# Kernel tuning notes

Hardware: AMD Instinct MI355X
Metric: run time of the kernel (lower is better)

## Reference

```python
import jax, jax.numpy as jnp
import numpy as np

S, L, K = 4, 256, 32          # num_states, seq length, neighbors
ORIG_H, EMB_H, EXV, RANK = 128, 256, 384, 16


def _integrate(x, Wq, Wk, seq_idx, emb_idx, hidden, rank):
    """AttentionIntegrator.forward: QK^T softmax -> double mean -> softmax -> weighted pool of raw x."""
    x = jnp.moveaxis(x, (seq_idx, emb_idx), (-2, -1))
    orig_shape = x.shape
    Ls = orig_shape[-2]
    xf = x.reshape(-1, Ls, hidden)               # (B, Ls, hidden)
    B = xf.shape[0]
    q = (xf @ Wq.T).reshape(B, Ls, rank, hidden)  # head_dim == hidden
    k = (xf @ Wk.T).reshape(B, Ls, rank, hidden)
    scale = 1.0 / jnp.sqrt(jnp.asarray(hidden, xf.dtype))
    scores = jnp.einsum('blhd,bmhd->bhlm', q, k) * scale
    attn = jax.nn.softmax(scores, axis=-1)        # (B, rank, Ls, Ls)
    w = jax.nn.softmax(attn.mean(axis=(1, 2)), axis=-1)  # (B, Ls)
    pooled = jnp.einsum('bl,bld->bd', w, xf)      # (B, hidden)
    return (pooled.reshape(*orig_shape[:-2], hidden),
            w.reshape(*orig_shape[:-2], Ls))


def setup_inputs() -> dict:
    key = jax.random.key(0)
    ks = jax.random.split(key, 12)
    sc = lambda fan_in: 1.0 / np.sqrt(fan_in)
    return {
        'h_V':    jax.random.normal(ks[0], (S, L, ORIG_H), jnp.float32),
        'h_EXV':  jax.random.normal(ks[1], (S, L, K, EXV), jnp.float32),
        'W_hV':   jax.random.normal(ks[2], (EMB_H, ORIG_H), jnp.float32) * sc(ORIG_H),
        'b_hV':   jnp.zeros((EMB_H,), jnp.float32),
        'Wq_hv':  jax.random.normal(ks[3], (RANK * EMB_H, EMB_H), jnp.float32) * sc(EMB_H),
        'Wk_hv':  jax.random.normal(ks[4], (RANK * EMB_H, EMB_H), jnp.float32) * sc(EMB_H),
        'Wq_ce':  jax.random.normal(ks[5], (RANK * EXV, EXV), jnp.float32) * sc(EXV),
        'Wk_ce':  jax.random.normal(ks[6], (RANK * EXV, EXV), jnp.float32) * sc(EXV),
        'W_ce':   jax.random.normal(ks[7], (EMB_H, EXV), jnp.float32) * sc(EXV),
        'b_ce':   jnp.zeros((EMB_H,), jnp.float32),
        'Wq_sce': jax.random.normal(ks[8], (RANK * EMB_H, EMB_H), jnp.float32) * sc(EMB_H),
        'Wk_sce': jax.random.normal(ks[9], (RANK * EMB_H, EMB_H), jnp.float32) * sc(EMB_H),
    }


def reference(h_V, h_EXV, W_hV, b_hV, Wq_hv, Wk_hv, Wq_ce, Wk_ce, W_ce, b_ce, Wq_sce, Wk_sce):
    # diffmodel.get_weights
    hv = h_V @ W_hV.T + b_hV                                  # (S, L, EMB_H)
    h_V_int, h_V_w = _integrate(hv, Wq_hv, Wk_hv, 0, 2, EMB_H, RANK)   # pool over states
    # chemical environment: pool over k neighbors per (state, position)
    ce, _local_w = _integrate(h_EXV, Wq_ce, Wk_ce, 2, 3, EXV, RANK)    # (S, L, EXV)
    ce = ce @ W_ce.T + b_ce                                   # (S, L, EMB_H)
    ce_int, ce_w = _integrate(ce, Wq_sce, Wk_sce, 0, 2, EMB_H, RANK)   # pool over states
    return (h_V_int[None], h_V_w[None], ce_int[None], ce_w[None])
```

## Files before the change

kernel.cpp:

```cpp
#include <hip/hip_runtime.h>

typedef _Float16 f16;
typedef _Float16 f16x8 __attribute__((ext_vector_type(8)));
typedef _Float16 f16x4 __attribute__((ext_vector_type(4)));
typedef float f32x4 __attribute__((ext_vector_type(4)));

#define MFMA16(a, b, c) __builtin_amdgcn_mfma_f32_16x16x32_f16(a, b, c, 0, 0, 0)
#define MFMA16K16(a, b, c) __builtin_amdgcn_mfma_f32_16x16x16f16(a, b, c, 0, 0, 0)

__global__ __launch_bounds__(256) void k_mt3(const float* __restrict__ Wq_hv,
                                             const float* __restrict__ Wk_hv,
                                             f16* __restrict__ mt_hv,
                                             const float* __restrict__ Wq_ce,
                                             const float* __restrict__ Wk_ce,
                                             f16* __restrict__ mt_ce,
                                             const float* __restrict__ Wq_sce,
                                             const float* __restrict__ Wk_sce,
                                             f16* __restrict__ mt_sce) {
    const int y = blockIdx.y;
    const float *Wq, *Wk;
    f16* MT;
    int H, ty;
    if (y < 16)      { Wq = Wq_hv;  Wk = Wk_hv;  MT = mt_hv;  H = 256; ty = y; }
    else if (y < 52) { Wq = Wq_ce;  Wk = Wk_ce;  MT = mt_ce;  H = 384; ty = y - 16; }
    else             { Wq = Wq_sce; Wk = Wk_sce; MT = mt_sce; H = 256; ty = y - 52; }

    const int h = blockIdx.x;
    const int ntile = H >> 6;
    const int nkk = H >> 5;
    const int frow = (ty / ntile) * 64;
    const int ecol = (ty % ntile) * 64;
    const int t = threadIdx.x;
    const int lane = t & 63;
    const int w = t >> 6;
    const int wr = w >> 1, wc = w & 1;

    __shared__ __align__(16) f16 As[64][40];
    __shared__ __align__(16) f16 Ks[64][40];

    f32x4 acc[2][2] = {};
    const int d = t >> 3;
    const int e8 = (t & 7) * 8;

    for (int kk = 0; kk < nkk; ++kk) {
        const float* gq = Wq + (size_t)(h * H + kk * 32 + d) * H + ecol + e8;
        const float* gk = Wk + (size_t)(h * H + kk * 32 + d) * H + frow + e8;
        float q[8], k[8];
#pragma unroll
        for (int i = 0; i < 8; ++i) { q[i] = gq[i]; k[i] = gk[i]; }
        __syncthreads();
#pragma unroll
        for (int i = 0; i < 8; ++i) { As[e8 + i][d] = (f16)q[i]; Ks[e8 + i][d] = (f16)k[i]; }
        __syncthreads();
        f16x8 a[2], b[2];
#pragma unroll
        for (int rt = 0; rt < 2; ++rt)
            a[rt] = *(const f16x8*)&Ks[wr * 32 + rt * 16 + (lane & 15)][(lane >> 4) * 8];
#pragma unroll
        for (int nt = 0; nt < 2; ++nt)
            b[nt] = *(const f16x8*)&As[wc * 32 + nt * 16 + (lane & 15)][(lane >> 4) * 8];
#pragma unroll
        for (int rt = 0; rt < 2; ++rt)
#pragma unroll
            for (int nt = 0; nt < 2; ++nt)
                acc[rt][nt] = MFMA16(a[rt], b[nt], acc[rt][nt]);
    }
#pragma unroll
    for (int rt = 0; rt < 2; ++rt)
#pragma unroll
        for (int nt = 0; nt < 2; ++nt)
#pragma unroll
            for (int j = 0; j < 4; ++j) {
                int f = frow + wr * 32 + rt * 16 + (lane >> 4) * 4 + j;
                int e = ecol + wc * 32 + nt * 16 + (lane & 15);
                MT[(((size_t)h * nkk + (e >> 5)) * H + f) * 32 + (e & 31)] = (f16)acc[rt][nt][j];
            }
}

__global__ __launch_bounds__(256) void k_lin(const float* __restrict__ in,
                                             const float* __restrict__ W,
                                             const float* __restrict__ bias,
                                             float* __restrict__ out, int K) {
    const int t = threadIdx.x;
    const int r0 = blockIdx.x * 4;
    __shared__ float ins[4][384];
    __shared__ float Ws[256][33];
#pragma unroll
    for (int r = 0; r < 4; ++r)
        for (int off = t; off < K; off += 256)
            ins[r][off] = in[(size_t)(r0 + r) * K + off];
    float acc[4] = {};
    for (int d0 = 0; d0 < K; d0 += 32) {
        __syncthreads();
        for (int i = t; i < 256 * 32; i += 256) {
            int j = i >> 5, dd = i & 31;
            Ws[j][dd] = W[(size_t)j * K + d0 + dd];
        }
        __syncthreads();
#pragma unroll 8
        for (int dd = 0; dd < 32; ++dd) {
            float wv = Ws[t][dd];
#pragma unroll
            for (int r = 0; r < 4; ++r) acc[r] += wv * ins[r][d0 + dd];
        }
    }
    float bv = bias[t];
#pragma unroll
    for (int r = 0; r < 4; ++r) out[(size_t)(r0 + r) * 256 + t] = acc[r] + bv;
}

__global__ __launch_bounds__(256) void k_small_int(const float* __restrict__ X,
                                                   const f16* __restrict__ MT,
                                                   float* __restrict__ wpart) {
    const int t = threadIdx.x;
    const int lane = t & 63;
    const int w = t >> 6;
    const int g = lane >> 4;
    const int l15 = lane & 15;
    const int pos0 = blockIdx.x * 8;
    const int h = blockIdx.y;

    __shared__ __align__(16) f16 Xs[32][264];
    __shared__ __align__(16) f16 Ts[32][264];

    {
        int row = t >> 3, d0 = (t & 7) * 32;
        int s = row & 3, p = row >> 2;
        const float* gx = X + (size_t)(s * 256 + pos0 + p) * 256 + d0;
#pragma unroll
        for (int i = 0; i < 32; i += 8) {
            float4 v0 = *(const float4*)(gx + i);
            float4 v1 = *(const float4*)(gx + i + 4);
            f16x8 o;
            o[0] = (f16)v0.x; o[1] = (f16)v0.y; o[2] = (f16)v0.z; o[3] = (f16)v0.w;
            o[4] = (f16)v1.x; o[5] = (f16)v1.y; o[6] = (f16)v1.z; o[7] = (f16)v1.w;
            *(f16x8*)&Xs[row][d0 + i] = o;
        }
    }
    __syncthreads();

    const f16* mh = MT + (size_t)h * 8 * 256 * 32;
    const int fb = w * 64 + l15;
    f32x4 acc[2][4] = {};
    f16x8 bq[4], bn[4];
#pragma unroll
    for (int nt = 0; nt < 4; ++nt)
        bq[nt] = *(const f16x8*)(mh + (size_t)(fb + nt * 16) * 32 + g * 8);
#pragma unroll
    for (int kk = 0; kk < 8; ++kk) {
        if (kk < 7) {
#pragma unroll
            for (int nt = 0; nt < 4; ++nt)
                bn[nt] = *(const f16x8*)(mh + ((size_t)(kk + 1) * 256 + fb + nt * 16) * 32 + g * 8);
        }
        f16x8 a[2];
#pragma unroll
        for (int mt = 0; mt < 2; ++mt)
            a[mt] = *(const f16x8*)&Xs[mt * 16 + l15][kk * 32 + g * 8];
#pragma unroll
        for (int mt = 0; mt < 2; ++mt)
#pragma unroll
            for (int nt = 0; nt < 4; ++nt)
                acc[mt][nt] = MFMA16(a[mt], bq[nt], acc[mt][nt]);
#pragma unroll
        for (int nt = 0; nt < 4; ++nt) bq[nt] = bn[nt];
    }
#pragma unroll
    for (int mt = 0; mt < 2; ++mt)
#pragma unroll
        for (int nt = 0; nt < 4; ++nt)
#pragma unroll
            for (int j = 0; j < 4; ++j)
                Ts[mt * 16 + g * 4 + j][w * 64 + nt * 16 + l15] = (f16)acc[mt][nt][j];
    __syncthreads();

    if (w < 2) {
        f32x4 sacc = {};
#pragma unroll
        for (int ks = 0; ks < 8; ++ks) {
            f16x8 a = *(const f16x8*)&Ts[w * 16 + l15][ks * 32 + g * 8];
            f16x8 b = *(const f16x8*)&Xs[w * 16 + l15][ks * 32 + g * 8];
            sacc = MFMA16(a, b, sacc);
        }
        if ((l15 >> 2) == g) {
            const float scale = 1.0f / 16.0f;
            float add = 0.f;
#pragma unroll
            for (int j = 0; j < 4; ++j) {
                float v = sacc[j] * scale;
                float m = v;
                m = fmaxf(m, __shfl_xor(m, 1));
                m = fmaxf(m, __shfl_xor(m, 2));
                float e = expf(v - m);
                float s2 = e;
                s2 += __shfl_xor(s2, 1);
                s2 += __shfl_xor(s2, 2);
                add += e / s2;
            }
            int pg = pos0 + w * 4 + g;
            wpart[((size_t)h * 256 + pg) * 4 + (l15 & 3)] = add;
        }
    }
}

__global__ __launch_bounds__(256) void k_small_fin(const float* __restrict__ wpart,
                                                   const float* __restrict__ X,
                                                   float* __restrict__ out_int,
                                                   float* __restrict__ out_w) {
    const int pos = blockIdx.x, t = threadIdx.x;
    __shared__ float red[64];
    __shared__ float ws[4];
    if (t < 64) red[t] = wpart[((size_t)(t >> 2) * 256 + pos) * 4 + (t & 3)];
    __syncthreads();
    if (t == 0) {
        float v[4];
#pragma unroll
        for (int s = 0; s < 4; ++s) {
            float x = 0.f;
            for (int hh = 0; hh < 16; ++hh) x += red[hh * 4 + s];
            v[s] = x * (1.0f / 64.0f);
        }
        float m = fmaxf(fmaxf(v[0], v[1]), fmaxf(v[2], v[3]));
        float sum = 0.f;
#pragma unroll
        for (int s = 0; s < 4; ++s) { v[s] = expf(v[s] - m); sum += v[s]; }
#pragma unroll
        for (int s = 0; s < 4; ++s) ws[s] = v[s] / sum;
    }
    __syncthreads();
    if (t < 4) out_w[pos * 4 + t] = ws[t];
    float v = 0.f;
#pragma unroll
    for (int s = 0; s < 4; ++s) v += ws[s] * X[(size_t)(s * 256 + pos) * 256 + t];
    out_int[(size_t)pos * 256 + t] = v;
}

#define BUF_OFF 98304

__global__ __launch_bounds__(512, 2) void k_ce_int(const float* __restrict__ Xg32,
                                                   const f16* __restrict__ MT,
                                                   float* __restrict__ acc_out) {
    const int t = threadIdx.x;
    const int lane = t & 63;
    const int w = t >> 6;
    const int g = lane >> 4;
    const int l15 = lane & 15;
    const int bg = blockIdx.x;

    extern __shared__ __align__(16) char smem[];
    char* BUF = smem + BUF_OFF;

    {
        const float* xg = Xg32 + (size_t)bg * 128 * 384;
#pragma unroll
        for (int p = 0; p < 12; ++p) {
            int idx = p * 512 + t;
            int row = idx / 48, s = idx - row * 48;
            int c = s ^ (row & 7);
            const float* src = xg + row * 384 + c * 8;
            float4 v0 = *(const float4*)src;
            float4 v1 = *(const float4*)(src + 4);
            f16x8 o;
            o[0] = (f16)v0.x; o[1] = (f16)v0.y; o[2] = (f16)v0.z; o[3] = (f16)v0.w;
            o[4] = (f16)v1.x; o[5] = (f16)v1.y; o[6] = (f16)v1.z; o[7] = (f16)v1.w;
            *(f16x8*)(smem + idx * 16) = o;
        }
    }
    __syncthreads();

    const f16* mall = MT;
    const int frow = w * 48 + l15;

    f16x8 A[3][3];
#pragma unroll
    for (int ft = 0; ft < 3; ++ft) {
        A[0][ft] = *(const f16x8*)(mall + (size_t)(frow + ft * 16) * 32 + g * 8);
        A[1][ft] = *(const f16x8*)(mall + (size_t)12288 + (size_t)(frow + ft * 16) * 32 + g * 8);
    }

    for (int hi = 0; hi < 16; ++hi) {
        f32x4 acc[3][8] = {};
#pragma unroll
        for (int kk = 0; kk < 12; ++kk) {
            {
                int step = hi * 12 + kk + 2;
                int ns = step < 192 ? step : 191;
#pragma unroll
                for (int ft = 0; ft < 3; ++ft)
                    A[(kk + 2) % 3][ft] =
                        *(const f16x8*)(mall + (size_t)ns * 12288 + (size_t)(frow + ft * 16) * 32 + g * 8);
            }
            f16x8 xb[8];
#pragma unroll
            for (int mt = 0; mt < 8; ++mt) {
                int row = mt * 16 + l15;
                int ch = kk * 4 + g;
                xb[mt] = *(const f16x8*)(smem + row * 768 + ((ch ^ (row & 7)) << 4));
            }
            __builtin_amdgcn_s_setprio(1);
#pragma unroll
            for (int ft = 0; ft < 3; ++ft)
#pragma unroll
                for (int mt = 0; mt < 8; ++mt)
                    acc[ft][mt] = MFMA16(A[kk % 3][ft], xb[mt], acc[ft][mt]);
            __builtin_amdgcn_s_setprio(0);
        }

        f16x4 bf[3][8];
#pragma unroll
        for (int ft = 0; ft < 3; ++ft)
#pragma unroll
            for (int mt = 0; mt < 8; ++mt) {
                f32x4 v = acc[ft][mt];
                f16x4 o;
                o[0] = (f16)v[0]; o[1] = (f16)v[1]; o[2] = (f16)v[2]; o[3] = (f16)v[3];
                bf[ft][mt] = o;
            }

#pragma unroll
        for (int r = 0; r < 2; ++r) {
            f32x4 s2[2][2][2] = {};
#pragma unroll
            for (int bb = 0; bb < 2; ++bb) {
                const int b = 2 * r + bb;
#pragma unroll
                for (int ks = 0; ks < 3; ++ks)
#pragma unroll
                    for (int it = 0; it < 2; ++it) {
                        int row = b * 32 + it * 16 + l15;
                        int ch = 6 * w + 2 * ks + (g >> 1);
                        f16x4 av = *(const f16x4*)(smem + row * 768 +
                                                   ((ch ^ (row & 7)) << 4) + 8 * (g & 1));
#pragma unroll
                        for (int lt = 0; lt < 2; ++lt)
                            s2[bb][it][lt] = MFMA16K16(av, bf[ks][2 * b + lt], s2[bb][it][lt]);
                    }
            }
#pragma unroll
            for (int bb = 0; bb < 2; ++bb)
#pragma unroll
                for (int it = 0; it < 2; ++it)
#pragma unroll
                    for (int lt = 0; lt < 2; ++lt)
                        *(f32x4*)(BUF + w * 8192 + (bb * 4 + it * 2 + lt) * 1024 + lane * 16) =
                            s2[bb][it][lt];
            __syncthreads();

            if ((w >> 2) == r) {
                const int wl = w & 3;
                const int bb = wl >> 1;
                const int it = wl & 1;
                const int b = 2 * r + bb;
                f32x4 sum0 = {0.f, 0.f, 0.f, 0.f};
                f32x4 sum1 = {0.f, 0.f, 0.f, 0.f};
#pragma unroll
                for (int src = 0; src < 8; ++src) {
                    const char* pb = BUF + src * 8192 + (bb * 4 + it * 2) * 1024 + lane * 16;
                    sum0 += *(const f32x4*)pb;
                    sum1 += *(const f32x4*)(pb + 1024);
                }
                const float scale = 0.051031036307982884f;
                float cs0 = 0.f, cs1 = 0.f;
#pragma unroll
                for (int j = 0; j < 4; ++j) {
                    float v0 = sum0[j] * scale, v1 = sum1[j] * scale;
                    float m = fmaxf(v0, v1);
                    m = fmaxf(m, __shfl_xor(m, 1));
                    m = fmaxf(m, __shfl_xor(m, 2));
                    m = fmaxf(m, __shfl_xor(m, 4));
                    m = fmaxf(m, __shfl_xor(m, 8));
                    float e0 = expf(v0 - m), e1 = expf(v1 - m);
                    float s = e0 + e1;
                    s += __shfl_xor(s, 1);
                    s += __shfl_xor(s, 2);
                    s += __shfl_xor(s, 4);
                    s += __shfl_xor(s, 8);
                    float inv = 1.f / s;
                    cs0 += e0 * inv;
                    cs1 += e1 * inv;
                }
                cs0 += __shfl_xor(cs0, 16); cs0 += __shfl_xor(cs0, 32);
                cs1 += __shfl_xor(cs1, 16); cs1 += __shfl_xor(cs1, 32);
                if (lane < 16) {
                    float* o = acc_out + (((size_t)hi * 1024 + bg * 4 + b) * 2 + it) * 32;
                    o[l15] = cs0;
                    o[16 + l15] = cs1;
                }
            }
            __syncthreads();
        }
    }
}

__global__ __launch_bounds__(128) void k_ce_pool(const float* __restrict__ accp,
                                                 const float* __restrict__ exv,
                                                 float* __restrict__ pooled) {
    const int b = blockIdx.x;
    const int t = threadIdx.x;
    __shared__ float wm[32];
    __shared__ float ww[32];
    if (t < 32) {
        float s = 0.f;
#pragma unroll
        for (int h = 0; h < 16; ++h) {
            s += accp[(((size_t)h * 1024 + b) * 2 + 0) * 32 + t];
            s += accp[(((size_t)h * 1024 + b) * 2 + 1) * 32 + t];
        }
        wm[t] = s * (1.0f / 512.0f);
    }
    __syncthreads();
    if (t == 0) {
        float m = wm[0];
        for (int i = 1; i < 32; ++i) m = fmaxf(m, wm[i]);
        float s = 0.f;
        for (int i = 0; i < 32; ++i) { float e = expf(wm[i] - m); ww[i] = e; s += e; }
        float inv = 1.f / s;
        for (int i = 0; i < 32; ++i) ww[i] *= inv;
    }
    __syncthreads();
    for (int d = t; d < 384; d += 128) {
        float v = 0.f;
#pragma unroll
        for (int m = 0; m < 32; ++m) v += ww[m] * exv[((size_t)b * 32 + m) * 384 + d];
        pooled[(size_t)b * 384 + d] = v;
    }
}

extern "C" void kernel_launch(void* const* d_in, const int* in_sizes, int n_in,
                              void* d_out, int out_size, void* d_ws, size_t ws_size,
                              hipStream_t stream) {
    const float* h_V    = (const float*)d_in[0];
    const float* h_EXV  = (const float*)d_in[1];
    const float* W_hV   = (const float*)d_in[2];
    const float* b_hV   = (const float*)d_in[3];
    const float* Wq_hv  = (const float*)d_in[4];
    const float* Wk_hv  = (const float*)d_in[5];
    const float* Wq_ce  = (const float*)d_in[6];
    const float* Wk_ce  = (const float*)d_in[7];
    const float* W_ce   = (const float*)d_in[8];
    const float* b_ce   = (const float*)d_in[9];
    const float* Wq_sce = (const float*)d_in[10];
    const float* Wk_sce = (const float*)d_in[11];
    float* out = (float*)d_out;

    char* ws = (char*)d_ws;
    f16*   mt_hv  = (f16*)(ws + 0);
    f16*   mt_sce = (f16*)(ws + 2097152);
    f16*   mt_ce  = (f16*)(ws + 4194304);
    float* hv     = (float*)(ws + 8912896);
    float* ce     = (float*)(ws + 9961472);
    float* accp   = (float*)(ws + 11010048);
    float* pooled = (float*)(ws + 15204352);
    float* wpart  = accp;

    k_mt3<<<dim3(16, 68), 256, 0, stream>>>(Wq_hv, Wk_hv, mt_hv,
                                            Wq_ce, Wk_ce, mt_ce,
                                            Wq_sce, Wk_sce, mt_sce);
    k_lin<<<256, 256, 0, stream>>>(h_V, W_hV, b_hV, hv, 128);
    k_small_int<<<dim3(32, 16), 256, 0, stream>>>(hv, mt_hv, wpart);
    k_small_fin<<<256, 256, 0, stream>>>(wpart, hv, out + 0, out + 65536);
    k_ce_int<<<dim3(256), 512, 163840, stream>>>(h_EXV, mt_ce, accp);
    k_ce_pool<<<1024, 128, 0, stream>>>(accp, h_EXV, pooled);
    k_lin<<<256, 256, 0, stream>>>(pooled, W_ce, b_ce, ce, 384);
    k_small_int<<<dim3(32, 16), 256, 0, stream>>>(ce, mt_sce, wpart);
    k_small_fin<<<256, 256, 0, stream>>>(wpart, ce, out + 66560, out + 132096);
}
```

Before: 301.9 us.

## Halve ce_int tile to 64 rows, store partial scores in fp16, double grid

```diff
diff --git a/kernel.cpp b/kernel.cpp
--- a/kernel.cpp
+++ b/kernel.cpp
@@ -235,7 +235,7 @@
     out_int[(size_t)pos * 256 + t] = v;
 }
 
-#define BUF_OFF 98304
+#define BUF_OFF 49152
 
 __global__ __launch_bounds__(512, 2) void k_ce_int(const float* __restrict__ Xg32,
                                                    const f16* __restrict__ MT,
@@ -251,9 +251,9 @@
     char* BUF = smem + BUF_OFF;
 
     {
-        const float* xg = Xg32 + (size_t)bg * 128 * 384;
-#pragma unroll
-        for (int p = 0; p < 12; ++p) {
+        const float* xg = Xg32 + (size_t)bg * 64 * 384;
+#pragma unroll
+        for (int p = 0; p < 6; ++p) {
             int idx = p * 512 + t;
             int row = idx / 48, s = idx - row * 48;
             int c = s ^ (row & 7);
@@ -279,7 +279,7 @@
     }
 
     for (int hi = 0; hi < 16; ++hi) {
-        f32x4 acc[3][8] = {};
+        f32x4 acc[3][4] = {};
 #pragma unroll
         for (int kk = 0; kk < 12; ++kk) {
             {
@@ -290,9 +290,9 @@
                     A[(kk + 2) % 3][ft] =
                         *(const f16x8*)(mall + (size_t)ns * 12288 + (size_t)(frow + ft * 16) * 32 + g * 8);
             }
-            f16x8 xb[8];
-#pragma unroll
-            for (int mt = 0; mt < 8; ++mt) {
+            f16x8 xb[4];
+#pragma unroll
+            for (int mt = 0; mt < 4; ++mt) {
                 int row = mt * 16 + l15;
                 int ch = kk * 4 + g;
                 xb[mt] = *(const f16x8*)(smem + row * 768 + ((ch ^ (row & 7)) << 4));
@@ -301,75 +301,69 @@
 #pragma unroll
             for (int ft = 0; ft < 3; ++ft)
 #pragma unroll
-                for (int mt = 0; mt < 8; ++mt)
+                for (int mt = 0; mt < 4; ++mt)
                     acc[ft][mt] = MFMA16(A[kk % 3][ft], xb[mt], acc[ft][mt]);
             __builtin_amdgcn_s_setprio(0);
         }
 
-        f16x4 bf[3][8];
+        f16x4 bf[3][4];
 #pragma unroll
         for (int ft = 0; ft < 3; ++ft)
 #pragma unroll
-            for (int mt = 0; mt < 8; ++mt) {
+            for (int mt = 0; mt < 4; ++mt) {
                 f32x4 v = acc[ft][mt];
                 f16x4 o;
                 o[0] = (f16)v[0]; o[1] = (f16)v[1]; o[2] = (f16)v[2]; o[3] = (f16)v[3];
                 bf[ft][mt] = o;
             }
 
+        const float scale = 0.051031036307982884f;
+
 #pragma unroll
         for (int r = 0; r < 2; ++r) {
-            f32x4 s2[2][2][2] = {};
-#pragma unroll
-            for (int bb = 0; bb < 2; ++bb) {
-                const int b = 2 * r + bb;
-#pragma unroll
-                for (int ks = 0; ks < 3; ++ks)
-#pragma unroll
-                    for (int it = 0; it < 2; ++it) {
-                        int row = b * 32 + it * 16 + l15;
-                        int ch = 6 * w + 2 * ks + (g >> 1);
-                        f16x4 av = *(const f16x4*)(smem + row * 768 +
-                                                   ((ch ^ (row & 7)) << 4) + 8 * (g & 1));
-#pragma unroll
-                        for (int lt = 0; lt < 2; ++lt)
-                            s2[bb][it][lt] = MFMA16K16(av, bf[ks][2 * b + lt], s2[bb][it][lt]);
-                    }
-            }
-#pragma unroll
-            for (int bb = 0; bb < 2; ++bb)
-#pragma unroll
-                for (int it = 0; it < 2; ++it)
+            f32x4 s2[2][2] = {};
+#pragma unroll
+            for (int ks = 0; ks < 3; ++ks)
+#pragma unroll
+                for (int it = 0; it < 2; ++it) {
+                    int row = r * 32 + it * 16 + l15;
+                    int ch = 6 * w + 2 * ks + (g >> 1);
+                    f16x4 av = *(const f16x4*)(smem + row * 768 +
+                                               ((ch ^ (row & 7)) << 4) + 8 * (g & 1));
 #pragma unroll
                     for (int lt = 0; lt < 2; ++lt)
-                        *(f32x4*)(BUF + w * 8192 + (bb * 4 + it * 2 + lt) * 1024 + lane * 16) =
-                            s2[bb][it][lt];
+                        s2[it][lt] = MFMA16K16(av, bf[ks][r * 2 + lt], s2[it][lt]);
+                }
+#pragma unroll
+            for (int it = 0; it < 2; ++it)
+#pragma unroll
+                for (int lt = 0; lt < 2; ++lt) {
+                    f16x4 p;
+#pragma unroll
+                    for (int j = 0; j < 4; ++j) p[j] = (f16)(s2[it][lt][j] * scale);
+                    *(f16x4*)(BUF + w * 2048 + (it * 2 + lt) * 512 + lane * 8) = p;
+                }
             __syncthreads();
 
-            if ((w >> 2) == r) {
-                const int wl = w & 3;
-                const int bb = wl >> 1;
-                const int it = wl & 1;
-                const int b = 2 * r + bb;
-                f32x4 sum0 = {0.f, 0.f, 0.f, 0.f};
-                f32x4 sum1 = {0.f, 0.f, 0.f, 0.f};
+            if (w < 2) {
+                f16x4 s0 = {(f16)0, (f16)0, (f16)0, (f16)0};
+                f16x4 s1 = {(f16)0, (f16)0, (f16)0, (f16)0};
 #pragma unroll
                 for (int src = 0; src < 8; ++src) {
-                    const char* pb = BUF + src * 8192 + (bb * 4 + it * 2) * 1024 + lane * 16;
-                    sum0 += *(const f32x4*)pb;
-                    sum1 += *(const f32x4*)(pb + 1024);
+                    const char* pb = BUF + src * 2048 + (w * 2) * 512 + lane * 8;
+                    s0 += *(const f16x4*)pb;
+                    s1 += *(const f16x4*)(pb + 512);
                 }
-                const float scale = 0.051031036307982884f;
                 float cs0 = 0.f, cs1 = 0.f;
 #pragma unroll
                 for (int j = 0; j < 4; ++j) {
-                    float v0 = sum0[j] * scale, v1 = sum1[j] * scale;
+                    float v0 = (float)s0[j], v1 = (float)s1[j];
                     float m = fmaxf(v0, v1);
                     m = fmaxf(m, __shfl_xor(m, 1));
                     m = fmaxf(m, __shfl_xor(m, 2));
                     m = fmaxf(m, __shfl_xor(m, 4));
                     m = fmaxf(m, __shfl_xor(m, 8));
-                    float e0 = expf(v0 - m), e1 = expf(v1 - m);
+                    float e0 = __expf(v0 - m), e1 = __expf(v1 - m);
                     float s = e0 + e1;
                     s += __shfl_xor(s, 1);
                     s += __shfl_xor(s, 2);
@@ -382,7 +376,7 @@
                 cs0 += __shfl_xor(cs0, 16); cs0 += __shfl_xor(cs0, 32);
                 cs1 += __shfl_xor(cs1, 16); cs1 += __shfl_xor(cs1, 32);
                 if (lane < 16) {
-                    float* o = acc_out + (((size_t)hi * 1024 + bg * 4 + b) * 2 + it) * 32;
+                    float* o = acc_out + (((size_t)hi * 1024 + bg * 2 + r) * 2 + w) * 32;
                     o[l15] = cs0;
                     o[16 + l15] = cs1;
                 }
@@ -459,7 +453,7 @@
     k_lin<<<256, 256, 0, stream>>>(h_V, W_hV, b_hV, hv, 128);
     k_small_int<<<dim3(32, 16), 256, 0, stream>>>(hv, mt_hv, wpart);
     k_small_fin<<<256, 256, 0, stream>>>(wpart, hv, out + 0, out + 65536);
-    k_ce_int<<<dim3(256), 512, 163840, stream>>>(h_EXV, mt_ce, accp);
+    k_ce_int<<<dim3(512), 512, 65536, stream>>>(h_EXV, mt_ce, accp);
     k_ce_pool<<<1024, 128, 0, stream>>>(accp, h_EXV, pooled);
     k_lin<<<256, 256, 0, stream>>>(pooled, W_ce, b_ce, ce, 384);
     k_small_int<<<dim3(32, 16), 256, 0, stream>>>(ce, mt_sce, wpart);
```

Result: slower. 356.6 us (+18.1%).
